# Performance work log

Hardware: AMD Instinct MI355X
Metric: run time of the kernel (lower is better)

## Reference

```python
import jax, jax.numpy as jnp
import numpy as np

N_NODES = 100000
N_EDGES = 1600000
H = 64
EPS_SM = 1e-16
NEG_SLOPE = 0.01  # LeakyReLU default
BN_EPS = 1e-5


def leaky_relu(x):
    return jnp.where(x >= 0, x, NEG_SLOPE * x)


def transformer_conv(x, src, tgt, edge_attr, Wq, bq, Wk, bk, Wv, bv, We, Ws, bs):
    # PyG TransformerConv, heads=1, concat=True, root_weight=True, lin_edge bias=False
    n = x.shape[0]
    q = x @ Wq + bq            # [N,H]
    k = x @ Wk + bk            # [N,H]
    v = x @ Wv + bv            # [N,H]
    e = edge_attr @ We         # [E,H]
    ke = k[src] + e            # [E,H]
    score = jnp.sum(q[tgt] * ke, axis=-1) / jnp.sqrt(jnp.float32(H))  # [E]
    # segment softmax over incoming edges of each target node
    m = jax.ops.segment_max(score, tgt, num_segments=n)
    m = jnp.where(jnp.isfinite(m), m, 0.0)
    p = jnp.exp(score - m[tgt])
    denom = jax.ops.segment_sum(p, tgt, num_segments=n)
    alpha = p / (denom[tgt] + EPS_SM)
    msg = (v[src] + e) * alpha[:, None]                  # [E,H]
    out = jax.ops.segment_sum(msg, tgt, num_segments=n)  # [N,H]
    return out + x @ Ws + bs


def batch_norm(x, gamma, beta):
    mean = jnp.mean(x, axis=0)
    var = jnp.mean((x - mean) ** 2, axis=0)
    return (x - mean) / jnp.sqrt(var + BN_EPS) * gamma + beta


def setup_inputs() -> dict:
    key = jax.random.key(0)
    ks = jax.random.split(key, 24)
    s = 0.05
    d = {
        "x": jax.random.normal(ks[0], (N_NODES, 2), jnp.float32),
        "edge_index": jax.random.randint(ks[1], (2, N_EDGES), 0, N_NODES, jnp.int32),
        "edge_attr": jax.random.normal(ks[2], (N_EDGES, 2), jnp.float32),
        "mask": jax.random.uniform(ks[3], (N_NODES,), jnp.float32),
        # gcn1 (in=2)
        "Wq1": jax.random.normal(ks[4], (2, H)) * s, "bq1": jnp.zeros((H,)),
        "Wk1": jax.random.normal(ks[5], (2, H)) * s, "bk1": jnp.zeros((H,)),
        "Wv1": jax.random.normal(ks[6], (2, H)) * s, "bv1": jnp.zeros((H,)),
        "We1": jax.random.normal(ks[7], (2, H)) * s,
        "Ws1": jax.random.normal(ks[8], (2, H)) * s, "bs1": jnp.zeros((H,)),
        # gcn2 (in=64)
        "Wq2": jax.random.normal(ks[9], (H, H)) * s, "bq2": jnp.zeros((H,)),
        "Wk2": jax.random.normal(ks[10], (H, H)) * s, "bk2": jnp.zeros((H,)),
        "Wv2": jax.random.normal(ks[11], (H, H)) * s, "bv2": jnp.zeros((H,)),
        "We2": jax.random.normal(ks[12], (2, H)) * s,
        "Ws2": jax.random.normal(ks[13], (H, H)) * s, "bs2": jnp.zeros((H,)),
        # batch norm
        "bn_gamma": jnp.ones((H,)), "bn_beta": jnp.zeros((H,)),
        # final MLP 64->32->1
        "Wf1": jax.random.normal(ks[14], (H, 32)) * s, "bf1": jnp.zeros((32,)),
        "Wf2": jax.random.normal(ks[15], (32, 1)) * s, "bf2": jnp.zeros((1,)),
        "iterations": 3,
    }
    return d


def reference(x, edge_index, edge_attr, mask,
              Wq1, bq1, Wk1, bk1, Wv1, bv1, We1, Ws1, bs1,
              Wq2, bq2, Wk2, bk2, Wv2, bv2, We2, Ws2, bs2,
              bn_gamma, bn_beta, Wf1, bf1, Wf2, bf2, iterations):
    src, tgt = edge_index[0], edge_index[1]
    h = transformer_conv(x, src, tgt, edge_attr, Wq1, bq1, Wk1, bk1, Wv1, bv1, We1, Ws1, bs1)
    h = leaky_relu(batch_norm(h, bn_gamma, bn_beta))
    h = leaky_relu(transformer_conv(h, src, tgt, edge_attr, Wq2, bq2, Wk2, bk2, Wv2, bv2, We2, Ws2, bs2))
    for _ in range(iterations - 1):
        h = leaky_relu(transformer_conv(h, src, tgt, edge_attr, Wq2, bq2, Wk2, bk2, Wv2, bv2, We2, Ws2, bs2))
    out = jnp.squeeze(leaky_relu(h @ Wf1 + bf1) @ Wf2 + bf2, axis=-1)  # [N]
    return out * mask
```

## Files before the change

### kernel.cpp

```cpp
#include <hip/hip_runtime.h>
#include <hip/hip_fp16.h>

#define N_NODES 100000
#define N_EDGES 1600000
#define SCAN_B ((N_NODES + 1023) / 1024)
#define BSHIFT 7
#define NB_BKT ((N_NODES + 127) / 128)
#define BCAP 2560

typedef _Float16 half2_t __attribute__((ext_vector_type(2)));
typedef _Float16 half8_t __attribute__((ext_vector_type(8)));
typedef float f32x4 __attribute__((ext_vector_type(4)));

__device__ __forceinline__ float lrelu(float x) { return x >= 0.f ? x : 0.01f * x; }

__global__ void k_count(const int* __restrict__ tgt, int* __restrict__ deg) {
    int i = blockIdx.x * 256 + threadIdx.x;
    atomicAdd(&deg[tgt[i]], 1);
}

__global__ void k_scan1(const int* __restrict__ deg, int* __restrict__ bsum) {
    __shared__ int s[256];
    int t = threadIdx.x;
    int gi = blockIdx.x * 1024 + t * 4;
    int v = 0;
    if (gi < N_NODES) {
        int4 d = *(const int4*)&deg[gi];
        v = d.x + d.y + d.z + d.w;
    }
    s[t] = v;
    __syncthreads();
    for (int d = 128; d > 0; d >>= 1) {
        if (t < d) s[t] += s[t + d];
        __syncthreads();
    }
    if (t == 0) bsum[blockIdx.x] = s[0];
}

__global__ void k_scan2(int* bsum, int* rowptr) {
    if (threadIdx.x == 0) {
        int run = 0;
        for (int b = 0; b < SCAN_B; b++) {
            int v = bsum[b];
            bsum[b] = run;
            run += v;
        }
        rowptr[N_NODES] = run;
    }
}

__global__ void k_scan3(const int* __restrict__ deg, const int* __restrict__ bsum,
                        int* __restrict__ rowptr, int* __restrict__ fill) {
    __shared__ int s[256];
    int t = threadIdx.x;
    int gi = blockIdx.x * 1024 + t * 4;
    int4 d = make_int4(0, 0, 0, 0);
    if (gi < N_NODES) d = *(const int4*)&deg[gi];
    int tsum = d.x + d.y + d.z + d.w;
    s[t] = tsum;
    __syncthreads();
    for (int dd = 1; dd < 256; dd <<= 1) {
        int val = (t >= dd) ? s[t - dd] : 0;
        __syncthreads();
        s[t] += val;
        __syncthreads();
    }
    int texcl = s[t] - tsum + bsum[blockIdx.x];
    if (gi < N_NODES) {
        int4 w;
        w.x = texcl;
        w.y = texcl + d.x;
        w.z = texcl + d.x + d.y;
        w.w = texcl + d.x + d.y + d.z;
        *(int4*)&rowptr[gi] = w;
        *(int4*)&fill[gi] = w;
    }
}

__global__ void k_scatter(const int* __restrict__ src, const int* __restrict__ tgt,
                          const float2* __restrict__ ea,
                          int* __restrict__ fill, int2* __restrict__ csr) {
    int i = blockIdx.x * 256 + threadIdx.x;
    int t = tgt[i];
    float2 e = ea[i];
    int pos = atomicAdd(&fill[t], 1);
    __half2 h2 = __floats2half2_rn(e.x, e.y);
    csr[pos] = make_int2(src[i], *(int*)&h2);
}

__global__ __launch_bounds__(256) void k_bin1(const int* __restrict__ src,
                                              const int* __restrict__ tgt,
                                              const float2* __restrict__ ea,
                                              int* __restrict__ gCur,
                                              int2* __restrict__ bin) {
    __shared__ int hist[NB_BKT];
    __shared__ int cur[NB_BKT];
    int tid = threadIdx.x;
    for (int b = tid; b < NB_BKT; b += 256) hist[b] = 0;
    __syncthreads();
    int base = blockIdx.x * 6400;
#pragma unroll 5
    for (int k = 0; k < 25; k++) {
        int i = base + k * 256 + tid;
        atomicAdd(&hist[tgt[i] >> BSHIFT], 1);
    }
    __syncthreads();
    for (int b = tid; b < NB_BKT; b += 256)
        cur[b] = atomicAdd(&gCur[b], hist[b]);
    __syncthreads();
    for (int k = 0; k < 25; k++) {
        int i = base + k * 256 + tid;
        int t = tgt[i];
        int b = t >> BSHIFT;
        float2 e = ea[i];
        int pos = atomicAdd(&cur[b], 1);
        if (pos < BCAP) {
            __half2 h2 = __floats2half2_rn(e.x, e.y);
            int2 rec;
            rec.x = src[i] | ((t & 127) << 20);
            rec.y = *(int*)&h2;
            bin[(size_t)b * BCAP + pos] = rec;
        }
    }
}

__global__ __launch_bounds__(256) void k_bin2(const int* __restrict__ gCnt,
                                              const int2* __restrict__ bin,
                                              int2* __restrict__ csr,
                                              int* __restrict__ fill) {
    __shared__ int cnt[128];
    int tid = threadIdx.x;
    if (tid < 128) cnt[tid] = 0;
    __syncthreads();
    int b = blockIdx.x;
    int nb = min(gCnt[b], BCAP);
    const int2* myb = &bin[(size_t)b * BCAP];
    for (int i = tid; i < nb; i += 256) {
        int2 rec = myb[i];
        int tloc = (rec.x >> 20) & 127;
        int s = rec.x & 0xFFFFF;
        int pos = atomicAdd(&cnt[tloc], 1);
        if (pos < 64) {
            int node = (b << BSHIFT) + tloc;
            csr[((size_t)node << 6) + pos] = make_int2(s | (rec.x & 0xFFF00000), rec.y);
        }
    }
    __syncthreads();
    if (tid < 128) {
        int node = (b << BSHIFT) + tid;
        if (node < N_NODES) fill[node] = min(cnt[tid], 64);
    }
}

__global__ void k_prep2(const float* __restrict__ Wq, const float* __restrict__ Wk,
                        const float* __restrict__ Ws, const float* __restrict__ We,
                        const float* __restrict__ bk, float* __restrict__ Wcomb) {
    int idx = blockIdx.x * 256 + threadIdx.x;
    if (idx >= 9216) return;
    int j = idx / 144;
    int m = idx - j * 144;
    float v = 0.f;
    if (m < 64) {
        float s = 0.f;
        for (int ch = 0; ch < 64; ch++) s += Wq[j * 64 + ch] * Wk[m * 64 + ch];
        v = 0.125f * s;
    } else if (m < 128) {
        v = Ws[j * 64 + (m - 64)];
    } else if (m == 128) {
        float s = 0.f;
        for (int ch = 0; ch < 64; ch++) s += Wq[j * 64 + ch] * bk[ch];
        v = 0.125f * s;
    } else if (m <= 130) {
        float s = 0.f;
        for (int ch = 0; ch < 64; ch++) s += Wq[j * 64 + ch] * We[(m - 129) * 64 + ch];
        v = 0.125f * s;
    }
    Wcomb[idx] = v;
}

__global__ void k_prepb(const float* __restrict__ Wk2, const float* __restrict__ We2,
                        const float* __restrict__ bq2, const float* __restrict__ bk2,
                        const float* __restrict__ bs2, const float* __restrict__ Wq1,
                        const float* __restrict__ Wk1, const float* __restrict__ We1,
                        const float* __restrict__ bq1, const float* __restrict__ bk1,
                        float* __restrict__ bcomb) {
    int t = threadIdx.x;
    if (t >= 160) return;
    float v = 0.f;
    if (t < 64) {
        float s = 0.f;
        for (int i = 0; i < 64; i++) s += Wk2[t * 64 + i] * bq2[i];
        v = 0.125f * s;
    } else if (t < 128) {
        v = bs2[t - 64];
    } else if (t == 128) {
        float s = 0.f;
        for (int i = 0; i < 64; i++) s += bq2[i] * bk2[i];
        v = 0.125f * s;
    } else if (t <= 130) {
        float s = 0.f;
        for (int i = 0; i < 64; i++) s += bq2[i] * We2[(t - 129) * 64 + i];
        v = 0.125f * s;
    } else if (t < 144) {
        v = 0.f;
    } else {
        int t2 = t - 144;
        float s = 0.f;
        if (t2 < 4) {
            int j = t2 >> 1, m = t2 & 1;
            for (int ch = 0; ch < 64; ch++) s += Wq1[j * 64 + ch] * Wk1[m * 64 + ch];
        } else if (t2 < 6) {
            int j = t2 - 4;
            for (int ch = 0; ch < 64; ch++) s += Wq1[j * 64 + ch] * bk1[ch];
        } else if (t2 < 8) {
            int m = t2 - 6;
            for (int ch = 0; ch < 64; ch++) s += bq1[ch] * Wk1[m * 64 + ch];
        } else if (t2 == 8) {
            for (int ch = 0; ch < 64; ch++) s += bq1[ch] * bk1[ch];
        } else if (t2 < 13) {
            int j = (t2 - 9) >> 1, d = (t2 - 9) & 1;
            for (int ch = 0; ch < 64; ch++) s += Wq1[j * 64 + ch] * We1[d * 64 + ch];
        } else if (t2 < 15) {
            int d = t2 - 13;
            for (int ch = 0; ch < 64; ch++) s += bq1[ch] * We1[d * 64 + ch];
        }
        v = 0.125f * s;
    }
    bcomb[t] = v;
}

__global__ void k_prepw(const float* __restrict__ Wcomb, __half* __restrict__ wp) {
    int t = blockIdx.x * 256 + threadIdx.x;
    if (t >= 9216) return;
    int e = t & 7;
    int lane = (t >> 3) & 63;
    int kh = (t >> 9) & 1;
    int fm = t >> 10;
    int k = (kh << 5) + ((lane >> 4) << 3) + e;
    int c = fm * 16 + (lane & 15);
    wp[t] = __float2half(Wcomb[k * 144 + c]);
}

__global__ void k_prepv(const float* __restrict__ Wv, __half* __restrict__ wvp) {
    int t = blockIdx.x * 256 + threadIdx.x;
    if (t >= 4096) return;
    int e = t & 7;
    int lane = (t >> 3) & 63;
    int kh = (t >> 9) & 1;
    int fm = t >> 10;
    int k = (kh << 5) + ((lane >> 4) << 3) + e;
    int c = fm * 16 + (lane & 15);
    wvp[t] = __float2half(Wv[k * 64 + c]);
}

__global__ __launch_bounds__(256) void k_agg1(
    const float* __restrict__ x, const int* __restrict__ idx,
    const int2* __restrict__ csr, const float* __restrict__ Wv,
    const float* __restrict__ We, const float* __restrict__ Ws,
    const float* __restrict__ bv, const float* __restrict__ bs,
    const float* __restrict__ prep, float* __restrict__ o, int bucket) {
    int node = blockIdx.x * 4 + (threadIdx.x >> 6);
    int lane = threadIdx.x & 63;
    float2 xt = *(const float2*)&x[(size_t)node << 1];
    float a0 = xt.x * prep[0] + xt.y * prep[2] + prep[6];
    float a1 = xt.x * prep[1] + xt.y * prep[3] + prep[7];
    float b1 = xt.x * prep[4] + xt.y * prep[5] + prep[8];
    float g0 = xt.x * prep[9] + xt.y * prep[11] + prep[13];
    float g1 = xt.x * prep[10] + xt.y * prep[12] + prep[14];

    float l = 0.f, px0 = 0.f, px1 = 0.f, pA = 0.f, pB = 0.f;
    if (bucket) {
        int deg = idx[node];
        bool valid = lane < deg;
        int2 rec = valid ? csr[((size_t)node << 6) + lane] : make_int2(0, 0);
        int src = rec.x & 0xFFFFF;
        float2 ef = __half22float2(*(__half2*)&rec.y);
        float2 xs = valid ? *(const float2*)&x[(size_t)src << 1] : make_float2(0.f, 0.f);
        float t = a0 * xs.x + a1 * xs.y + b1 + g0 * ef.x + g1 * ef.y;
        float pp = valid ? __expf(t) : 0.f;
        l = pp;
        px0 = pp * xs.x;
        px1 = pp * xs.y;
        pA = pp * ef.x;
        pB = pp * ef.y;
    } else {
        int beg = idx[node], end = idx[node + 1];
        for (int p = beg + lane; p < end; p += 64) {
            int2 rec = csr[p];
            float2 ef = __half22float2(*(__half2*)&rec.y);
            float2 xs = *(const float2*)&x[(size_t)rec.x << 1];
            float t = a0 * xs.x + a1 * xs.y + b1 + g0 * ef.x + g1 * ef.y;
            float pp = __expf(t);
            l += pp;
            px0 += pp * xs.x;
            px1 += pp * xs.y;
            pA += pp * ef.x;
            pB += pp * ef.y;
        }
    }
#pragma unroll
    for (int D = 1; D < 64; D <<= 1) {
        l += __shfl_xor(l, D, 64);
        px0 += __shfl_xor(px0, D, 64);
        px1 += __shfl_xor(px1, D, 64);
        pA += __shfl_xor(pA, D, 64);
        pB += __shfl_xor(pB, D, 64);
    }
    float inv = 1.f / (l + 1e-16f);
    int c = lane;
    float r = (px0 * Wv[c] + px1 * Wv[64 + c] + pA * We[c] + pB * We[64 + c] +
               l * bv[c]) * inv +
              xt.x * Ws[c] + xt.y * Ws[64 + c] + bs[c];
    o[((size_t)node << 6) + c] = r;
}

__global__ void k_bnp(const float* __restrict__ o, float* __restrict__ bnsum,
                      float* __restrict__ bnsq) {
    __shared__ float s1[256], s2[256];
    int t = threadIdx.x;
    int c = t & 63, nsub = t >> 6;
    float su = 0.f, sq = 0.f;
    int base = blockIdx.x * 400;
    for (int i = 0; i < 100; i++) {
        int node = base + i * 4 + nsub;
        float v = o[((size_t)node << 6) + c];
        su += v;
        sq += v * v;
    }
    s1[t] = su;
    s2[t] = sq;
    __syncthreads();
    if (t < 64) {
        float a = s1[t] + s1[t + 64] + s1[t + 128] + s1[t + 192];
        float b = s2[t] + s2[t + 64] + s2[t + 128] + s2[t + 192];
        atomicAdd(&bnsum[t], a);
        atomicAdd(&bnsq[t], b);
    }
}

__global__ void k_bnf(const float* bnsum, const float* bnsq, const float* gamma,
                      const float* beta, float* bnab) {
    int c = threadIdx.x;
    float mean = bnsum[c] * (1.f / N_NODES);
    float var = bnsq[c] * (1.f / N_NODES) - mean * mean;
    float A = gamma[c] * rsqrtf(var + 1e-5f);
    bnab[c] = A;
    bnab[64 + c] = beta[c] - mean * A;
}

__global__ void k_bna(const float* __restrict__ o, const float* __restrict__ bnab,
                      float* __restrict__ h, __half* __restrict__ hh) {
    int idx = blockIdx.x * 256 + threadIdx.x;
    int c = idx & 63;
    float v = lrelu(o[idx] * bnab[c] + bnab[64 + c]);
    h[idx] = v;
    hh[idx] = __float2half(v);
}

__device__ __forceinline__ half8_t pack8(float4 lo, float4 hi) {
    half8_t r;
    r[0] = (_Float16)lo.x; r[1] = (_Float16)lo.y;
    r[2] = (_Float16)lo.z; r[3] = (_Float16)lo.w;
    r[4] = (_Float16)hi.x; r[5] = (_Float16)hi.y;
    r[6] = (_Float16)hi.z; r[7] = (_Float16)hi.w;
    return r;
}

__global__ __launch_bounds__(256) void k_gemm(
    const float* __restrict__ h, const __half* __restrict__ hhin,
    const __half* __restrict__ wp, const float* __restrict__ bcomb,
    const float* __restrict__ bnab, int use_bn,
    __half* __restrict__ qh, float* __restrict__ ext, __half* __restrict__ hhout) {
    __shared__ __half qsm[64 * 68];
    int tid = threadIdx.x;
    int w = tid >> 6;
    int lane = tid & 63;
    int nloc = lane & 15;
    int kg = lane >> 4;
    int base = blockIdx.x * 64;

    half8_t A[2], AE[2];
    const half8_t* wpv = (const half8_t*)wp;
#pragma unroll
    for (int kh = 0; kh < 2; kh++) A[kh] = wpv[((w << 1) + kh) * 64 + lane];
    if (w == 3) {
#pragma unroll
        for (int kh = 0; kh < 2; kh++) AE[kh] = wpv[((8 << 1) + kh) * 64 + lane];
    }

    half8_t z8;
#pragma unroll
    for (int i = 0; i < 8; i++) z8[i] = (_Float16)0.f;

    half8_t B[4][2];
    int n[4];
    bool g[4];
#pragma unroll
    for (int nf = 0; nf < 4; nf++) {
        n[nf] = base + (nf << 4) + nloc;
        g[nf] = n[nf] < N_NODES;
    }

    if (use_bn) {
        float4 bnA[2][2], bnB[2][2];
#pragma unroll
        for (int kh = 0; kh < 2; kh++) {
            int k0 = (kh << 5) + (kg << 3);
            bnA[kh][0] = *(const float4*)&bnab[k0];
            bnA[kh][1] = *(const float4*)&bnab[k0 + 4];
            bnB[kh][0] = *(const float4*)&bnab[64 + k0];
            bnB[kh][1] = *(const float4*)&bnab[64 + k0 + 4];
        }
        const float4 z4 = make_float4(0.f, 0.f, 0.f, 0.f);
#pragma unroll
        for (int nf = 0; nf < 4; nf++) {
            const float* hrow = h + ((size_t)n[nf] << 6);
#pragma unroll
            for (int kh = 0; kh < 2; kh++) {
                int k0 = (kh << 5) + (kg << 3);
                float4 lo = g[nf] ? *(const float4*)&hrow[k0] : z4;
                float4 hi = g[nf] ? *(const float4*)&hrow[k0 + 4] : z4;
                lo.x = lrelu(lo.x * bnA[kh][0].x + bnB[kh][0].x);
                lo.y = lrelu(lo.y * bnA[kh][0].y + bnB[kh][0].y);
                lo.z = lrelu(lo.z * bnA[kh][0].z + bnB[kh][0].z);
                lo.w = lrelu(lo.w * bnA[kh][0].w + bnB[kh][0].w);
                hi.x = lrelu(hi.x * bnA[kh][1].x + bnB[kh][1].x);
                hi.y = lrelu(hi.y * bnA[kh][1].y + bnB[kh][1].y);
                hi.z = lrelu(hi.z * bnA[kh][1].z + bnB[kh][1].z);
                hi.w = lrelu(hi.w * bnA[kh][1].w + bnB[kh][1].w);
                B[nf][kh] = pack8(lo, hi);
                if (g[nf]) *(half8_t*)&hhout[((size_t)n[nf] << 6) + k0] = B[nf][kh];
            }
        }
    } else {
#pragma unroll
        for (int nf = 0; nf < 4; nf++) {
#pragma unroll
            for (int kh = 0; kh < 2; kh++) {
                int k0 = (kh << 5) + (kg << 3);
                B[nf][kh] = g[nf] ? *(const half8_t*)&hhin[((size_t)n[nf] << 6) + k0]
                                  : z8;
            }
        }
    }

    f32x4 acc[4], accE[4];
#pragma unroll
    for (int nf = 0; nf < 4; nf++) {
        acc[nf] = (f32x4){0.f, 0.f, 0.f, 0.f};
        accE[nf] = (f32x4){0.f, 0.f, 0.f, 0.f};
    }

#pragma unroll
    for (int nf = 0; nf < 4; nf++) {
        acc[nf] = __builtin_amdgcn_mfma_f32_16x16x32_f16(A[0], B[nf][0], acc[nf],
                                                          0, 0, 0);
        acc[nf] = __builtin_amdgcn_mfma_f32_16x16x32_f16(A[1], B[nf][1], acc[nf],
                                                          0, 0, 0);
    }
    if (w == 3) {
#pragma unroll
        for (int nf = 0; nf < 4; nf++) {
            accE[nf] = __builtin_amdgcn_mfma_f32_16x16x32_f16(AE[0], B[nf][0],
                                                              accE[nf], 0, 0, 0);
            accE[nf] = __builtin_amdgcn_mfma_f32_16x16x32_f16(AE[1], B[nf][1],
                                                              accE[nf], 0, 0, 0);
        }
    }

    int rowg = kg << 2;
    int c0 = (w << 4) + rowg;
    float4 bi = *(const float4*)&bcomb[c0];
#pragma unroll
    for (int nf = 0; nf < 4; nf++) {
        int nl = (nf << 4) + nloc;
        __half2 p0 = __floats2half2_rn(acc[nf][0] + bi.x, acc[nf][1] + bi.y);
        __half2 p1 = __floats2half2_rn(acc[nf][2] + bi.z, acc[nf][3] + bi.w);
        *(__half2*)&qsm[nl * 68 + c0] = p0;
        *(__half2*)&qsm[nl * 68 + c0 + 2] = p1;
    }
    if (w == 3 && kg == 0) {
        float4 be = *(const float4*)&bcomb[128];
#pragma unroll
        for (int nf = 0; nf < 4; nf++) {
            if (!g[nf]) continue;
            float4 r;
            r.x = accE[nf][0] + be.x;
            r.y = accE[nf][1] + be.y;
            r.z = accE[nf][2] + be.z;
            r.w = accE[nf][3] + be.w;
            *(float4*)&ext[(size_t)n[nf] << 2] = r;
        }
    }
    __syncthreads();
#pragma unroll
    for (int rep = 0; rep < 8; rep++) {
        int i = rep * 256 + tid;
        int row = i >> 5;
        int col = (i & 31) << 1;
        if (base + row < N_NODES) {
            int v = *(int*)&qsm[row * 68 + col];
            *(int*)&qh[((size_t)(base + row) << 6) + col] = v;
        }
    }
}

__global__ __launch_bounds__(256) void k_aggH(
    const __half* __restrict__ qh, const float* __restrict__ ext,
    const __half* __restrict__ hh, const int* __restrict__ idx,
    const int2* __restrict__ csr, __half* __restrict__ Shat,
    float* __restrict__ svec, int bucket) {
    int tid = threadIdx.x;
    int wv = tid >> 6;
    int node = blockIdx.x * 4 + wv;
    int lane = tid & 63;
    int w = lane >> 4;
    int j = lane & 15;

    float4 ex = *(const float4*)&ext[(size_t)node << 2];
    float beta = ex.x, qe0 = ex.y, qe1 = ex.z;
    int2 qraw = *(const int2*)&qh[((size_t)node << 6) + (j << 2)];
    half2_t q01 = *(half2_t*)&qraw.x;
    half2_t q23 = *(half2_t*)&qraw.y;

    float l = 0.f, sA = 0.f, sB = 0.f;
    float4 acc = make_float4(0.f, 0.f, 0.f, 0.f);

    auto body = [&](int2 hraw, int cry, bool cvalid) {
        float2 ef = __half22float2(*(__half2*)&cry);
#if __has_builtin(__builtin_amdgcn_fdot2)
        half2_t h01 = *(half2_t*)&hraw.x;
        half2_t h23 = *(half2_t*)&hraw.y;
        float t = __builtin_amdgcn_fdot2(h01, q01,
                  __builtin_amdgcn_fdot2(h23, q23, 0.f, false), false);
#else
        float2 a01 = __half22float2(*(__half2*)&hraw.x);
        float2 a23 = __half22float2(*(__half2*)&hraw.y);
        float2 qa = __half22float2(*(__half2*)&qraw.x);
        float2 qb = __half22float2(*(__half2*)&qraw.y);
        float t = qa.x * a01.x + qa.y * a01.y + qb.x * a23.x + qb.y * a23.y;
#endif
#pragma unroll
        for (int off = 1; off < 16; off <<= 1) t += __shfl_xor(t, off, 64);
        t += beta + ef.x * qe0 + ef.y * qe1;
        float pp = cvalid ? __expf(t) : 0.f;
        float2 h01f = __half22float2(*(__half2*)&hraw.x);
        float2 h23f = __half22float2(*(__half2*)&hraw.y);
        l += pp;
        acc.x += pp * h01f.x;
        acc.y += pp * h01f.y;
        acc.z += pp * h23f.x;
        acc.w += pp * h23f.y;
        sA += pp * ef.x;
        sB += pp * ef.y;
    };

    if (bucket) {
        int deg = idx[node];
        int2 myrec = (lane < deg) ? csr[((size_t)node << 6) + lane] : make_int2(0, 0);
        int nIter = (deg + 3) >> 2;
        if (nIter > 0) {
            int es = (w < deg) ? w : 0;
            int rx = __shfl(myrec.x, es, 64) & 0xFFFFF;
            int ry = __shfl(myrec.y, es, 64);
            int2 raw = *(const int2*)&hh[((size_t)rx << 6) + (j << 2)];
            for (int i = 0; i < nIter; i++) {
                int2 craw = raw;
                int cry = ry;
                bool cvalid = (w + (i << 2)) < deg;
                if (i + 1 < nIter) {
                    int e2 = w + ((i + 1) << 2);
                    int es2 = (e2 < deg) ? e2 : 0;
                    rx = __shfl(myrec.x, es2, 64) & 0xFFFFF;
                    ry = __shfl(myrec.y, es2, 64);
                    raw = *(const int2*)&hh[((size_t)rx << 6) + (j << 2)];
                }
                body(craw, cry, cvalid);
            }
        }
    } else {
        int beg = idx[node], end = idx[node + 1];
        for (int p = beg + w; p < end; p += 4) {
            int2 rec = csr[p];
            int2 raw = *(const int2*)&hh[((size_t)rec.x << 6) + (j << 2)];
            body(raw, rec.y, true);
        }
    }

#pragma unroll
    for (int D = 16; D < 64; D <<= 1) {
        l += __shfl_xor(l, D, 64);
        acc.x += __shfl_xor(acc.x, D, 64);
        acc.y += __shfl_xor(acc.y, D, 64);
        acc.z += __shfl_xor(acc.z, D, 64);
        acc.w += __shfl_xor(acc.w, D, 64);
        sA += __shfl_xor(sA, D, 64);
        sB += __shfl_xor(sB, D, 64);
    }

    float inv = 1.f / (l + 1e-16f);
    float f0 = __shfl(acc.x * inv, lane >> 2, 64);
    float f1 = __shfl(acc.y * inv, lane >> 2, 64);
    float f2 = __shfl(acc.z * inv, lane >> 2, 64);
    float f3 = __shfl(acc.w * inv, lane >> 2, 64);
    int sel = lane & 3;
    float v = (sel == 0) ? f0 : (sel == 1) ? f1 : (sel == 2) ? f2 : f3;
    Shat[((size_t)node << 6) + lane] = __float2half(v);
    if (lane == 0)
        *(float4*)&svec[(size_t)node << 2] =
            make_float4(sA * inv, sB * inv, l * inv, 0.f);
}

__global__ __launch_bounds__(256) void k_proj(
    const __half* __restrict__ Shat, const float* __restrict__ svec,
    const __half* __restrict__ hh, const __half* __restrict__ wp,
    const __half* __restrict__ wvp, const float* __restrict__ We,
    const float* __restrict__ bv, const float* __restrict__ bcomb,
    float* __restrict__ hout, __half* __restrict__ hhout, int whh, int whout) {
    __shared__ float lds4[64 * 68];
    __half* hsm = (__half*)lds4;
    int tid = threadIdx.x;
    int w = tid >> 6;
    int lane = tid & 63;
    int nloc = lane & 15;
    int kg = lane >> 4;
    int base = blockIdx.x * 64;

    const half8_t* wv = (const half8_t*)wvp;
    const half8_t* wpv = (const half8_t*)wp;
    half8_t Av0 = wv[((w << 1) + 0) * 64 + lane];
    half8_t Av1 = wv[((w << 1) + 1) * 64 + lane];
    half8_t As0 = wpv[(((4 + w) << 1) + 0) * 64 + lane];
    half8_t As1 = wpv[(((4 + w) << 1) + 1) * 64 + lane];

    int rowg = kg << 2;
    int c0 = (w << 4) + rowg;
    float4 we0 = *(const float4*)&We[c0];
    float4 we1 = *(const float4*)&We[64 + c0];
    float4 bv4 = *(const float4*)&bv[c0];
    float4 bs4 = *(const float4*)&bcomb[64 + c0];

    half8_t z8;
#pragma unroll
    for (int i = 0; i < 8; i++) z8[i] = (_Float16)0.f;

#pragma unroll
    for (int nf = 0; nf < 4; nf++) {
        int n = base + (nf << 4) + nloc;
        bool g = n < N_NODES;
        const __half* srow = Shat + ((size_t)n << 6);
        const __half* hrow = hh + ((size_t)n << 6);
        half8_t Bs0 = g ? *(const half8_t*)&srow[(kg << 3)] : z8;
        half8_t Bs1 = g ? *(const half8_t*)&srow[32 + (kg << 3)] : z8;
        half8_t Bh0 = g ? *(const half8_t*)&hrow[(kg << 3)] : z8;
        half8_t Bh1 = g ? *(const half8_t*)&hrow[32 + (kg << 3)] : z8;

        f32x4 acc = (f32x4){0.f, 0.f, 0.f, 0.f};
        acc = __builtin_amdgcn_mfma_f32_16x16x32_f16(Av0, Bs0, acc, 0, 0, 0);
        acc = __builtin_amdgcn_mfma_f32_16x16x32_f16(Av1, Bs1, acc, 0, 0, 0);
        acc = __builtin_amdgcn_mfma_f32_16x16x32_f16(As0, Bh0, acc, 0, 0, 0);
        acc = __builtin_amdgcn_mfma_f32_16x16x32_f16(As1, Bh1, acc, 0, 0, 0);

        float4 sv = g ? *(const float4*)&svec[(size_t)n << 2]
                      : make_float4(0.f, 0.f, 0.f, 0.f);
        float4 r;
        r.x = lrelu(acc[0] + sv.x * we0.x + sv.y * we1.x + sv.z * bv4.x + bs4.x);
        r.y = lrelu(acc[1] + sv.x * we0.y + sv.y * we1.y + sv.z * bv4.y + bs4.y);
        r.z = lrelu(acc[2] + sv.x * we0.z + sv.y * we1.z + sv.z * bv4.z + bs4.z);
        r.w = lrelu(acc[3] + sv.x * we0.w + sv.y * we1.w + sv.z * bv4.w + bs4.w);

        int nl = (nf << 4) + nloc;
        if (whout) {
            *(float4*)&lds4[nl * 68 + c0] = r;
        } else {
            __half2 p0 = __floats2half2_rn(r.x, r.y);
            __half2 p1 = __floats2half2_rn(r.z, r.w);
            *(__half2*)&hsm[nl * 68 + c0] = p0;
            *(__half2*)&hsm[nl * 68 + c0 + 2] = p1;
        }
    }
    __syncthreads();
    if (whout) {
#pragma unroll
        for (int rep = 0; rep < 4; rep++) {
            int i = rep * 256 + tid;
            int row = i >> 4;
            int c4 = (i & 15) << 2;
            if (base + row < N_NODES) {
                float4 v = *(float4*)&lds4[row * 68 + c4];
                *(float4*)&hout[((size_t)(base + row) << 6) + c4] = v;
            }
        }
    } else {
#pragma unroll
        for (int rep = 0; rep < 8; rep++) {
            int i = rep * 256 + tid;
            int row = i >> 5;
            int col = (i & 31) << 1;
            if (base + row < N_NODES) {
                int v = *(int*)&hsm[row * 68 + col];
                *(int*)&hhout[((size_t)(base + row) << 6) + col] = v;
            }
        }
    }
}

__global__ __launch_bounds__(256) void k_mlp(const float* __restrict__ h,
                                             const float* __restrict__ Wf1,
                                             const float* __restrict__ bf1,
                                             const float* __restrict__ Wf2,
                                             const float* __restrict__ bf2v,
                                             const float* __restrict__ mask,
                                             float* __restrict__ out) {
    __shared__ float W1[64 * 32];
    __shared__ float W2[32];
    __shared__ float hsm[8][64];
    __shared__ float zs[256];
    int tid = threadIdx.x;
    for (int i = tid; i < 2048; i += 256) W1[i] = Wf1[i];
    if (tid < 32) W2[tid] = Wf2[tid];
    int base = blockIdx.x * 8;
    for (int i = tid; i < 512; i += 256) {
        int n = i >> 6, c = i & 63;
        hsm[n][c] = h[(base + n) * 64 + c];
    }
    __syncthreads();
    int n = tid >> 5, j = tid & 31;
    float acc = bf1[j];
    for (int c = 0; c < 64; c++) acc += hsm[n][c] * W1[c * 32 + j];
    zs[tid] = lrelu(acc) * W2[j];
    __syncthreads();
    if (j == 0) {
        int node = base + n;
        float r = bf2v[0];
        for (int jj = 0; jj < 32; jj++) r += zs[(n << 5) + jj];
        out[node] = r * mask[node];
    }
}

extern "C" void kernel_launch(void* const* d_in, const int* in_sizes, int n_in,
                              void* d_out, int out_size, void* d_ws, size_t ws_size,
                              hipStream_t stream) {
    const float* x = (const float*)d_in[0];
    const int* ei = (const int*)d_in[1];
    const float* ea = (const float*)d_in[2];
    const float* mask = (const float*)d_in[3];
    const float *Wq1 = (const float*)d_in[4], *bq1 = (const float*)d_in[5];
    const float *Wk1 = (const float*)d_in[6], *bk1 = (const float*)d_in[7];
    const float *Wv1 = (const float*)d_in[8], *bv1 = (const float*)d_in[9];
    const float *We1 = (const float*)d_in[10];
    const float *Ws1 = (const float*)d_in[11], *bs1 = (const float*)d_in[12];
    const float *Wq2 = (const float*)d_in[13], *bq2 = (const float*)d_in[14];
    const float *Wk2 = (const float*)d_in[15], *bk2 = (const float*)d_in[16];
    const float *Wv2 = (const float*)d_in[17], *bv2 = (const float*)d_in[18];
    const float *We2 = (const float*)d_in[19];
    const float *Ws2 = (const float*)d_in[20], *bs2 = (const float*)d_in[21];
    const float *gamma = (const float*)d_in[22], *beta = (const float*)d_in[23];
    const float *Wf1 = (const float*)d_in[24], *bf1 = (const float*)d_in[25];
    const float *Wf2 = (const float*)d_in[26], *bf2v = (const float*)d_in[27];
    float* out = (float*)d_out;

    const size_t bucket_need =
        (size_t)NB_BKT * BCAP * 8 + (size_t)N_NODES * 64 * 8 +
        (size_t)N_NODES * 64 * 4 * 2 + (size_t)N_NODES * 64 * 2 * 4 +
        (size_t)N_NODES * 16 * 2 + (size_t)N_NODES * 4 * 3 + (1 << 20);
    bool use_bucket = ws_size >= bucket_need;

    char* ws = (char*)d_ws;
    size_t off = 0;
    auto alloc = [&](size_t b) {
        size_t r = off;
        off += (b + 255) & ~(size_t)255;
        return r;
    };
    int* deg = (int*)(ws + alloc(N_NODES * 4));
    int* fill = (int*)(ws + alloc(N_NODES * 4));
    int* rowptr = (int*)(ws + alloc((N_NODES + 1) * 4));
    int* bsum = (int*)(ws + alloc(SCAN_B * 4));
    int* gCur = (int*)(ws + alloc(NB_BKT * 4));
    float* bnsum = (float*)(ws + alloc(64 * 4));
    float* bnsq = (float*)(ws + alloc(64 * 4));
    float* bnab = (float*)(ws + alloc(128 * 4));
    float* Wcomb = (float*)(ws + alloc(9216 * 4));
    float* bcomb = (float*)(ws + alloc(160 * 4));
    __half* wp = (__half*)(ws + alloc(9216 * 2));
    __half* wvp = (__half*)(ws + alloc(4096 * 2));
    float* ext = (float*)(ws + alloc((size_t)N_NODES * 16));
    float* svec = (float*)(ws + alloc((size_t)N_NODES * 16));
    int2* bin1 = (int2*)(ws + alloc(use_bucket ? (size_t)NB_BKT * BCAP * 8 : 256));
    int2* csr = (int2*)(ws + alloc(use_bucket ? (size_t)N_NODES * 64 * 8
                                              : (size_t)N_EDGES * 8));
    __half* qh = (__half*)(ws + alloc((size_t)N_NODES * 64 * 2));
    __half* Shat = (__half*)(ws + alloc((size_t)N_NODES * 64 * 2));
    __half* hh0 = (__half*)(ws + alloc((size_t)N_NODES * 64 * 2));
    __half* hh1 = (__half*)(ws + alloc((size_t)N_NODES * 64 * 2));
    float* hbuf = (float*)(ws + alloc((size_t)N_NODES * 64 * 4));
    float* obuf = (float*)(ws + alloc((size_t)N_NODES * 64 * 4));

    const int* srcI = ei;
    const int* tgtI = ei + N_EDGES;

    hipMemsetAsync(bnsum, 0, 64 * 4, stream);
    hipMemsetAsync(bnsq, 0, 64 * 4, stream);

    k_prep2<<<36, 256, 0, stream>>>(Wq2, Wk2, Ws2, We2, bk2, Wcomb);
    k_prepb<<<1, 192, 0, stream>>>(Wk2, We2, bq2, bk2, bs2, Wq1, Wk1, We1, bq1, bk1,
                                   bcomb);
    k_prepw<<<36, 256, 0, stream>>>(Wcomb, wp);
    k_prepv<<<16, 256, 0, stream>>>(Wv2, wvp);

    const int* aggIdx;
    if (use_bucket) {
        hipMemsetAsync(gCur, 0, NB_BKT * 4, stream);
        k_bin1<<<250, 256, 0, stream>>>(srcI, tgtI, (const float2*)ea, gCur, bin1);
        k_bin2<<<NB_BKT, 256, 0, stream>>>(gCur, bin1, csr, fill);
        aggIdx = fill;
    } else {
        hipMemsetAsync(deg, 0, N_NODES * 4, stream);
        k_count<<<N_EDGES / 256, 256, 0, stream>>>(tgtI, deg);
        k_scan1<<<SCAN_B, 256, 0, stream>>>(deg, bsum);
        k_scan2<<<1, 64, 0, stream>>>(bsum, rowptr);
        k_scan3<<<SCAN_B, 256, 0, stream>>>(deg, bsum, rowptr, fill);
        k_scatter<<<N_EDGES / 256, 256, 0, stream>>>(srcI, tgtI, (const float2*)ea,
                                                     fill, csr);
        aggIdx = rowptr;
    }
    int bkt = use_bucket ? 1 : 0;

    k_agg1<<<N_NODES / 4, 256, 0, stream>>>(x, aggIdx, csr, Wv1, We1, Ws1, bv1, bs1,
                                            bcomb + 144, obuf, bkt);
    k_bnp<<<250, 256, 0, stream>>>(obuf, bnsum, bnsq);
    k_bnf<<<1, 64, 0, stream>>>(bnsum, bnsq, gamma, beta, bnab);
    if (!use_bucket)
        k_bna<<<N_NODES * 64 / 256, 256, 0, stream>>>(obuf, bnab, hbuf, hh0);

    const int gemm_grid = (N_NODES + 63) / 64;
    for (int it = 0; it < 3; ++it) {
        int bnflag = (it == 0 && use_bucket) ? 1 : 0;
        const __half* hhG = (it == 1) ? hh1 : hh0;
        __half* hhP = (it == 0) ? hh1 : hh0;
        k_gemm<<<gemm_grid, 256, 0, stream>>>(obuf, hhG, wp, bcomb, bnab, bnflag,
                                              qh, ext, (__half*)hhG);
        k_aggH<<<N_NODES / 4, 256, 0, stream>>>(qh, ext, hhG, aggIdx, csr, Shat,
                                                svec, bkt);
        k_proj<<<gemm_grid, 256, 0, stream>>>(Shat, svec, hhG, wp, wvp, We2, bv2,
                                              bcomb, hbuf, hhP, (it < 2) ? 1 : 0,
                                              (it == 2) ? 1 : 0);
    }
    k_mlp<<<N_NODES / 8, 256, 0, stream>>>(hbuf, Wf1, bf1, Wf2, bf2v, mask, out);
}
```

Before: 570.2 us.

## Remap aggregation lanes to 4 lanes per edge with LDS channel reduction

The attention-aggregation kernel now gives each edge 4 lanes that each load 16 halves with int4 loads, so a wave covers 16 edges per step instead of 4. Each lane accumulates 16 channels in registers, and a per-wave LDS transpose-reduction sums across edges to form the output. The goal is fewer loop iterations and fewer shuffle steps for the average degree, plus wider memory transactions on the gathers. In exchange it needs more registers and a shared-memory buffer, and it relies on wave-local LDS ordering with no barrier.

```diff
diff --git a/kernel.cpp b/kernel.cpp
--- a/kernel.cpp
+++ b/kernel.cpp
@@ -510,102 +510,130 @@
     const __half* __restrict__ hh, const int* __restrict__ idx,
     const int2* __restrict__ csr, __half* __restrict__ Shat,
     float* __restrict__ svec, int bucket) {
+    __shared__ float red[4 * 64 * 20];
     int tid = threadIdx.x;
     int wv = tid >> 6;
     int node = blockIdx.x * 4 + wv;
     int lane = tid & 63;
-    int w = lane >> 4;
-    int j = lane & 15;
+    int es = lane >> 2;
+    int cl = lane & 3;
 
     float4 ex = *(const float4*)&ext[(size_t)node << 2];
     float beta = ex.x, qe0 = ex.y, qe1 = ex.z;
-    int2 qraw = *(const int2*)&qh[((size_t)node << 6) + (j << 2)];
-    half2_t q01 = *(half2_t*)&qraw.x;
-    half2_t q23 = *(half2_t*)&qraw.y;
+    int4 qr0 = *(const int4*)&qh[((size_t)node << 6) + (cl << 4)];
+    int4 qr1 = *(const int4*)&qh[((size_t)node << 6) + (cl << 4) + 8];
+    const half2_t* qp0 = (const half2_t*)&qr0;
+    const half2_t* qp1 = (const half2_t*)&qr1;
 
     float l = 0.f, sA = 0.f, sB = 0.f;
-    float4 acc = make_float4(0.f, 0.f, 0.f, 0.f);
-
-    auto body = [&](int2 hraw, int cry, bool cvalid) {
-        float2 ef = __half22float2(*(__half2*)&cry);
+    float accv[16];
+#pragma unroll
+    for (int c = 0; c < 16; c++) accv[c] = 0.f;
+
+    int nEdge, rbase;
+    if (bucket) {
+        nEdge = idx[node];
+        rbase = node << 6;
+    } else {
+        rbase = idx[node];
+        nEdge = idx[node + 1] - rbase;
+    }
+    int nIter = (nEdge + 15) >> 4;
+
+    auto body = [&](int4 h0, int4 h1, int2 rec, bool ok) {
+        const half2_t* hp0 = (const half2_t*)&h0;
+        const half2_t* hp1 = (const half2_t*)&h1;
+        float t = 0.f;
 #if __has_builtin(__builtin_amdgcn_fdot2)
-        half2_t h01 = *(half2_t*)&hraw.x;
-        half2_t h23 = *(half2_t*)&hraw.y;
-        float t = __builtin_amdgcn_fdot2(h01, q01,
-                  __builtin_amdgcn_fdot2(h23, q23, 0.f, false), false);
+#pragma unroll
+        for (int p = 0; p < 4; p++)
+            t = __builtin_amdgcn_fdot2(hp0[p], qp0[p], t, false);
+#pragma unroll
+        for (int p = 0; p < 4; p++)
+            t = __builtin_amdgcn_fdot2(hp1[p], qp1[p], t, false);
 #else
-        float2 a01 = __half22float2(*(__half2*)&hraw.x);
-        float2 a23 = __half22float2(*(__half2*)&hraw.y);
-        float2 qa = __half22float2(*(__half2*)&qraw.x);
-        float2 qb = __half22float2(*(__half2*)&qraw.y);
-        float t = qa.x * a01.x + qa.y * a01.y + qb.x * a23.x + qb.y * a23.y;
+        const __half* hq0 = (const __half*)&qr0;
+        const __half* hq1 = (const __half*)&qr1;
+        const __half* hh0 = (const __half*)&h0;
+        const __half* hh1 = (const __half*)&h1;
+#pragma unroll
+        for (int c = 0; c < 8; c++) t += __half2float(hh0[c]) * __half2float(hq0[c]);
+#pragma unroll
+        for (int c = 0; c < 8; c++) t += __half2float(hh1[c]) * __half2float(hq1[c]);
 #endif
-#pragma unroll
-        for (int off = 1; off < 16; off <<= 1) t += __shfl_xor(t, off, 64);
+        t += __shfl_xor(t, 1, 64);
+        t += __shfl_xor(t, 2, 64);
+        float2 ef = __half22float2(*(__half2*)&rec.y);
         t += beta + ef.x * qe0 + ef.y * qe1;
-        float pp = cvalid ? __expf(t) : 0.f;
-        float2 h01f = __half22float2(*(__half2*)&hraw.x);
-        float2 h23f = __half22float2(*(__half2*)&hraw.y);
+        float pp = ok ? __expf(t) : 0.f;
         l += pp;
-        acc.x += pp * h01f.x;
-        acc.y += pp * h01f.y;
-        acc.z += pp * h23f.x;
-        acc.w += pp * h23f.y;
         sA += pp * ef.x;
         sB += pp * ef.y;
+        const __half* hs0 = (const __half*)&h0;
+        const __half* hs1 = (const __half*)&h1;
+#pragma unroll
+        for (int c = 0; c < 8; c++) accv[c] += pp * __half2float(hs0[c]);
+#pragma unroll
+        for (int c = 0; c < 8; c++) accv[8 + c] += pp * __half2float(hs1[c]);
     };
 
     if (bucket) {
-        int deg = idx[node];
-        int2 myrec = (lane < deg) ? csr[((size_t)node << 6) + lane] : make_int2(0, 0);
-        int nIter = (deg + 3) >> 2;
+        int2 recs[4];
+#pragma unroll
+        for (int i = 0; i < 4; i++) {
+            int e = (i << 4) + es;
+            recs[i] = (e < nEdge) ? csr[(size_t)rbase + e] : make_int2(0, 0);
+        }
         if (nIter > 0) {
-            int es = (w < deg) ? w : 0;
-            int rx = __shfl(myrec.x, es, 64) & 0xFFFFF;
-            int ry = __shfl(myrec.y, es, 64);
-            int2 raw = *(const int2*)&hh[((size_t)rx << 6) + (j << 2)];
-            for (int i = 0; i < nIter; i++) {
-                int2 craw = raw;
-                int cry = ry;
-                bool cvalid = (w + (i << 2)) < deg;
-                if (i + 1 < nIter) {
-                    int e2 = w + ((i + 1) << 2);
-                    int es2 = (e2 < deg) ? e2 : 0;
-                    rx = __shfl(myrec.x, es2, 64) & 0xFFFFF;
-                    ry = __shfl(myrec.y, es2, 64);
-                    raw = *(const int2*)&hh[((size_t)rx << 6) + (j << 2)];
+            int src0 = recs[0].x & 0xFFFFF;
+            const __half* hr = hh + ((size_t)src0 << 6) + (cl << 4);
+            int4 h0c = *(const int4*)&hr[0];
+            int4 h1c = *(const int4*)&hr[8];
+#pragma unroll
+            for (int i = 0; i < 4; i++) {
+                if (i < nIter) {
+                    int4 h0 = h0c, h1 = h1c;
+                    if (i + 1 < nIter) {
+                        int srcn = recs[i + 1].x & 0xFFFFF;
+                        const __half* hrn = hh + ((size_t)srcn << 6) + (cl << 4);
+                        h0c = *(const int4*)&hrn[0];
+                        h1c = *(const int4*)&hrn[8];
+                    }
+                    body(h0, h1, recs[i], ((i << 4) + es) < nEdge);
                 }
-                body(craw, cry, cvalid);
             }
         }
     } else {
-        int beg = idx[node], end = idx[node + 1];
-        for (int p = beg + w; p < end; p += 4) {
-            int2 rec = csr[p];
-            int2 raw = *(const int2*)&hh[((size_t)rec.x << 6) + (j << 2)];
-            body(raw, rec.y, true);
-        }
-    }
-
-#pragma unroll
-    for (int D = 16; D < 64; D <<= 1) {
+        for (int i = 0; i < nIter; i++) {
+            int e = (i << 4) + es;
+            bool ok = e < nEdge;
+            int2 rec = ok ? csr[(size_t)rbase + e] : make_int2(0, 0);
+            int src = rec.x & 0xFFFFF;
+            const __half* hr = hh + ((size_t)src << 6) + (cl << 4);
+            int4 h0 = *(const int4*)&hr[0];
+            int4 h1 = *(const int4*)&hr[8];
+            body(h0, h1, rec, ok);
+        }
+    }
+
+#pragma unroll
+    for (int D = 4; D < 64; D <<= 1) {
         l += __shfl_xor(l, D, 64);
-        acc.x += __shfl_xor(acc.x, D, 64);
-        acc.y += __shfl_xor(acc.y, D, 64);
-        acc.z += __shfl_xor(acc.z, D, 64);
-        acc.w += __shfl_xor(acc.w, D, 64);
         sA += __shfl_xor(sA, D, 64);
         sB += __shfl_xor(sB, D, 64);
     }
-
     float inv = 1.f / (l + 1e-16f);
-    float f0 = __shfl(acc.x * inv, lane >> 2, 64);
-    float f1 = __shfl(acc.y * inv, lane >> 2, 64);
-    float f2 = __shfl(acc.z * inv, lane >> 2, 64);
-    float f3 = __shfl(acc.w * inv, lane >> 2, 64);
-    int sel = lane & 3;
-    float v = (sel == 0) ? f0 : (sel == 1) ? f1 : (sel == 2) ? f2 : f3;
-    Shat[((size_t)node << 6) + lane] = __float2half(v);
+
+    float* my = &red[(wv * 64 + lane) * 20];
+#pragma unroll
+    for (int c = 0; c < 16; c += 4)
+        *(float4*)&my[c] = make_float4(accv[c], accv[c + 1], accv[c + 2], accv[c + 3]);
+    __asm__ volatile("" ::: "memory");
+    float s = 0.f;
+    int rb = wv * 64 * 20 + (lane >> 4) * 20 + (lane & 15);
+#pragma unroll
+    for (int es2 = 0; es2 < 16; es2++) s += red[rb + es2 * 80];
+    Shat[((size_t)node << 6) + lane] = __float2half(s * inv);
     if (lane == 0)
         *(float4*)&svec[(size_t)node << 2] =
             make_float4(sA * inv, sB * inv, l * inv, 0.f);
```

Measured after the change: 571.5 us. No clear change (+0.2%).
